# Kernel optimization log

Hardware: AMD Instinct MI355X
Metric: run time of the kernel (lower is better)

The kernel has to match this reference:

```python
import jax, jax.numpy as jnp
import numpy as np

B, V, D, E, F, H, HD = 16, 1024, 16, 64, 16, 128, 64
GRAPH_LAYERS, FLOW_ITERS, DUAL_ITERS = 2, 10, 10
STEP, MOM, BIG = 0.01, 0.9, 1e9


def _build_graph():
    # circulant graph: node v's d-th out-neighbor is v + offs[d] (mod V); offsets paired (o, -o)
    offs = np.array([1, -1, 2, -2, 3, -3, 4, -4, 5, -5, 6, -6, 7, -7, 8, -8], dtype=np.int32)
    v = np.arange(V, dtype=np.int32)[:, None]
    d = np.broadcast_to(np.arange(D, dtype=np.int32)[None, :], (V, D))
    adj = ((v + offs[None, :]) % V).astype(np.int32)
    inv_adj = ((v - offs[None, :]) % V).astype(np.int32)
    in_idx = np.stack([inv_adj, d], axis=-1)    # d-th incoming edge of v == out-edge (inv_adj[v,d], slot d)
    rev_idx = np.stack([adj, d], axis=-1)       # out-edge (v,d) is the d-th incoming edge of adj[v,d]
    opp_idx = np.stack([adj, d ^ 1], axis=-1)   # opposite edge (w->v) is slot d^1 at w (paired offsets)
    bt = lambda x: jnp.asarray(np.broadcast_to(x[None], (B,) + x.shape).copy())
    return bt(adj), bt(inv_adj), bt(in_idx), bt(rev_idx), bt(opp_idx)


def setup_inputs() -> dict:
    key = jax.random.key(0)
    ks = jax.random.split(key, 16)
    adj_lst, inv_adj_lst, in_indices, rev_indices, opp_indices = _build_graph()
    rn = lambda k, shape, scale=1.0: jax.random.normal(k, shape, dtype=jnp.float32) * scale
    s = lambda fan: 1.0 / float(np.sqrt(fan))
    return {
        'demands': rn(ks[0], (B, V, 1)),
        'node_features': rn(ks[1], (B, V, F)),
        'edge_lengths': jax.random.uniform(ks[2], (B, V, D), dtype=jnp.float32),
        'norm_edge_lengths': jax.random.uniform(ks[3], (B, V, D), dtype=jnp.float32),
        'node_emb': rn(ks[4], (V, E)),
        'W_enc': rn(ks[5], (E + F, H), s(E + F)), 'b_enc': jnp.zeros((H,), jnp.float32),
        'W_gat': rn(ks[6], (H, H), s(H)), 'b_gat': jnp.zeros((H,), jnp.float32),
        'a_gat': rn(ks[7], (H,), s(H)),
        'W_gru_x': rn(ks[8], (H, 3 * H), s(H)), 'W_gru_h': rn(ks[9], (H, 3 * H), s(H)),
        'b_gru': jnp.zeros((3 * H,), jnp.float32),
        'W_dec1': rn(ks[10], (2 * H, HD), s(2 * H)), 'b_dec1': jnp.zeros((HD,), jnp.float32),
        'W_dec2': rn(ks[11], (HD, 1), s(HD)), 'b_dec2': jnp.zeros((1,), jnp.float32),
        'W_dual1': rn(ks[12], (H, HD), s(H)), 'b_dual1': jnp.zeros((HD,), jnp.float32),
        'W_dual2': rn(ks[13], (HD, 1), s(HD)), 'b_dual2': jnp.zeros((1,), jnp.float32),
        'adj_lst': adj_lst, 'inv_adj_lst': inv_adj_lst,
        'in_indices': in_indices, 'rev_indices': rev_indices, 'opp_indices': opp_indices,
        'num_nodes': jnp.full((B,), V, dtype=jnp.int32),
    }


def _gather_nodes(values, idx, valid):
    # masked_gather with set_zero=True: values (B,V,H), idx (B,V,D) -> (B,V,D,H)
    bb = jnp.arange(values.shape[0])[:, None, None]
    g = values[bb, jnp.clip(idx, 0, values.shape[1] - 1)]
    return g * valid[..., None]


def _gather_edges(x, idx):
    # gather_nd into a (B,V,D,...) tensor; idx (B,V,D,2) = (node, slot), batch implicit
    bb = jnp.arange(x.shape[0])[:, None, None]
    return x[bb, idx[..., 0], idx[..., 1]]


def _sparsemax(z):
    n = z.shape[-1]
    zs = jnp.sort(z, axis=-1)[..., ::-1]
    k = jnp.arange(1, n + 1, dtype=z.dtype)
    zc = jnp.cumsum(zs, axis=-1)
    support = (1.0 + k * zs) > zc
    kz = jnp.sum(support, axis=-1, keepdims=True)
    tau = (jnp.take_along_axis(zc, kz - 1, axis=-1) - 1.0) / kz.astype(z.dtype)
    return jnp.maximum(z - tau, 0.0)


def _forward(demands, node_features, edge_lengths, norm_edge_lengths, node_emb, W_enc, b_enc,
             W_gat, b_gat, a_gat, W_gru_x, W_gru_h, b_gru, W_dec1, b_dec1, W_dec2, b_dec2,
             W_dual1, b_dual1, W_dual2, b_dual2,
             adj_lst, inv_adj_lst, in_indices, rev_indices, opp_indices, num_nodes):
    f32 = jnp.float32
    # embedding lookup with max_norm=1
    nrm = jnp.linalg.norm(node_emb, axis=-1, keepdims=True)
    emb = node_emb / jnp.maximum(nrm, 1.0)
    emb_b = jnp.broadcast_to(emb[None], (demands.shape[0], V, E))
    node_enc = jnp.concatenate([emb_b, node_features], axis=-1) @ W_enc + b_enc   # (B,V,H)
    mask = (adj_lst == num_nodes[:, None, None]).astype(f32)                       # 1 = padded slot
    valid = 1.0 - mask
    initial = _gather_nodes(node_enc, adj_lst, valid)                              # (B,V,D,H)
    h = initial
    for _ in range(GRAPH_LAYERS):
        # DirectionalGAT: per-edge transform, masked attention over slots, directional regather
        t = jnp.tanh(h @ W_gat + b_gat)                                            # (B,V,D,H)
        logits = jnp.einsum('bvdh,h->bvd', t, a_gat) - BIG * mask
        attn = jax.nn.softmax(logits, axis=-1)
        node_msg = jnp.einsum('bvd,bvdh->bvh', attn, t)                            # (B,V,H)
        msg = _gather_nodes(node_msg, adj_lst, valid)
        x = jnp.tanh(msg + initial)
        # GRU cell, shared weights over all edge states
        gx = x @ W_gru_x + b_gru
        gh = h @ W_gru_h
        z = jax.nn.sigmoid(gx[..., :H] + gh[..., :H])
        r = jax.nn.sigmoid(gx[..., H:2 * H] + gh[..., H:2 * H])
        cand = jnp.tanh(gx[..., 2 * H:] + r * gh[..., 2 * H:])
        h = z * h + (1.0 - z) * cand
    # decoder over (encoding, encoding + opposite-edge encoding)
    comb = h + _gather_edges(h, opp_indices)
    dec_in = jnp.concatenate([h, comb], axis=-1)
    nw = (jnp.tanh(dec_in @ W_dec1 + b_dec1) @ W_dec2 + b_dec2)[..., 0]            # (B,V,D)
    # destination attention: normalize over incoming edges, map back to outgoing layout
    inv_mask = (inv_adj_lst == num_nodes[:, None, None]).astype(f32)
    in_w = _gather_edges(nw, in_indices)
    dest_attn = jax.nn.softmax(in_w - BIG * inv_mask, axis=-1)
    nw = _gather_edges(dest_attn, rev_indices)
    pred = nw - BIG * mask
    normalized = _sparsemax(pred) * valid
    # iterative proportional min-cost-flow solver
    def mcf_step(flow, _):
        inflow = jnp.sum(_gather_edges(flow, in_indices), axis=-1, keepdims=True)  # (B,V,1)
        return normalized * jax.nn.relu(inflow - demands), None
    flow, _ = jax.lax.scan(mcf_step, jnp.zeros_like(normalized), None, length=FLOW_ITERS)
    flow_cost = jnp.sum(flow * flow, axis=(1, 2))                                  # square cost fn
    # dual variables + dual flow (projected momentum gradient descent)
    node_states = jnp.sum(h, axis=2)                                               # (B,V,H)
    dual_vars = jax.nn.relu(jnp.tanh(node_states @ W_dual1 + b_dual1) @ W_dual2 + b_dual2)  # (B,V,1)
    dual = mask * dual_vars
    dual_tr = _gather_nodes(dual_vars, adj_lst, valid)[..., 0]
    dual_diff = dual_tr - dual                                                     # (B,V,D)
    def dual_step(carry, _):
        f, vel = carry
        grad = 2.0 * f + dual_diff                                                 # d/df [f^2 + dual_diff*f]
        vel = MOM * vel - STEP * grad
        f = jax.nn.relu(f + vel)
        return (f, vel), None
    (dual_flows, _), _ = jax.lax.scan(dual_step, (jnp.zeros_like(dual_diff), jnp.zeros_like(dual_diff)), None, length=DUAL_ITERS)
    dual_flows = dual_flows * valid
    dual_demand = jnp.sum(dual_vars * demands, axis=(1, 2))
    dual_cost = jnp.sum(dual_flows * dual_flows + dual_diff * dual_flows, axis=(1, 2)) - dual_demand
    return flow_cost - dual_cost                                                   # (B,) primal-dual gap loss


def reference(demands, node_features, edge_lengths, norm_edge_lengths, node_emb, W_enc, b_enc,
              W_gat, b_gat, a_gat, W_gru_x, W_gru_h, b_gru, W_dec1, b_dec1, W_dec2, b_dec2,
              W_dual1, b_dual1, W_dual2, b_dual2,
              adj_lst, inv_adj_lst, in_indices, rev_indices, opp_indices, num_nodes):
    return _forward(demands, node_features, edge_lengths, norm_edge_lengths, node_emb, W_enc, b_enc,
                    W_gat, b_gat, a_gat, W_gru_x, W_gru_h, b_gru, W_dec1, b_dec1, W_dec2, b_dec2,
                    W_dual1, b_dual1, W_dual2, b_dual2,
                    adj_lst, inv_adj_lst, in_indices, rev_indices, opp_indices, num_nodes)
```

## Files before the change

### kernel.cpp

```cpp
#include <hip/hip_runtime.h>
#include <hip/hip_bf16.h>

#define B 16
#define V 1024
#define D 16
#define E 64
#define F 16
#define H 128
#define HD 64
#define BV (B*V)
#define BVD (B*V*D)

#define OFF_HNB      0
#define OFF_NORM     (OFF_HNB + BV*H/2)
#define OFF_DV       (OFF_NORM + BVD)
#define OFF_WT       (OFF_DV + BV)
#define OFF_WTG      (OFF_WT + 65536)
#define OFF_WPQ      (OFF_WTG + 8192)
#define OFF_WU1T     (OFF_WPQ + 8192)
#define OFF_WENCT    (OFF_WU1T + 4096)

typedef __attribute__((ext_vector_type(8))) short bf16x8;
typedef __attribute__((ext_vector_type(4))) float f32x4;

// ... 9 lines not shown
__device__ __forceinline__ float fsig(float x){ return frcp(1.f + __expf(-x)); }
__device__ __forceinline__ float ftanh(float x){
  float e = __expf(-2.f*fabsf(x));
  float r = (1.f - e)*frcp(1.f + e);
  return copysignf(r, x);
}

__global__ __launch_bounds__(256) void k_pre(const float* __restrict__ Wx, const float* __restrict__ Wh,
    const float* __restrict__ Wg, const float* __restrict__ W1, const float* __restrict__ Wu1,
    const float* __restrict__ Wenc,
    short* __restrict__ Wt, short* __restrict__ Wgt, short* __restrict__ Wpq,
    short* __restrict__ Wu1t, short* __restrict__ Wenct, float* __restrict__ outz){
  int bid = blockIdx.x, tid = threadIdx.x;
  if (bid == 0 && tid < 16) outz[tid] = 0.f;
  if (bid < 512){
    int n = bid, k = tid;
    int g = n >> 7, j = n & 127;
    float v;
    if (g == 0)      v = (k < 128) ? Wx[k*384 + j]       : Wh[(k-128)*384 + j];
    else if (g == 1) v = (k < 128) ? Wx[k*384 + 128 + j] : Wh[(k-128)*384 + 128 + j];
    else if (g == 2) v = (k < 128) ? Wx[k*384 + 256 + j] : 0.f;
    else             v = (k < 128) ? 0.f                 : Wh[(k-128)*384 + 256 + j];
    Wt[n*256 + k] = f2bf(v);
    return;
  }
  if (bid < 576){
    int idx = (bid-512)*256 + tid;
    int n = idx >> 7, k = idx & 127;
    Wgt[n*128 + k] = f2bf(Wg[k*128 + n]);
    return;
  }
  if (bid < 608){
    int idx = (bid-576)*256 + tid;
    int n = idx >> 7, k = idx & 127;
    float wb = W1[(k+128)*HD + n];
    float wa = W1[k*HD + n];
    Wpq[n*128 + k]      = f2bf(wa + wb);
    Wpq[(64+n)*128 + k] = f2bf(wb);
    return;
  }
  if (bid < 640){
    int idx = (bid-608)*256 + tid;
    int n = idx >> 7, k = idx & 127;
    Wu1t[n*128 + k] = f2bf(Wu1[k*HD + n]);
    return;
  }
  {
    int nn = (bid-640)*2 + (tid >> 7);
    int kk = tid & 127;
    if (kk < 96) Wenct[nn*96 + kk] = f2bf(kk < 80 ? Wenc[kk*128 + nn] : 0.f);
  }
}

__global__ __launch_bounds__(512,4) void k_mega(const float* __restrict__ emb, const float* __restrict__ nf,
    const short* __restrict__ Wenct, const float* __restrict__ benc, const int* __restrict__ adj,
    const short* __restrict__ Wgt, const float* __restrict__ bg, const float* __restrict__ ag,
    const short* __restrict__ Wt, const float* __restrict__ bgru, short* __restrict__ hout){
  __shared__ short NE[64][136];
  __shared__ short T[64][136];
  __shared__ short H1[48][136];
  __shared__ short X[48][136];
  __shared__ float Lp[8][64];
  __shared__ float Ls[64];
  __shared__ float nrmv[64];
  short (*As)[136] = T;

  int tid = threadIdx.x;
  int blk = blockIdx.x;
  int b = blk >> 5;
  int n0 = (blk & 31) << 5;
  int w = tid >> 6, lane = tid & 63;
  int l15 = lane & 15, quad = lane >> 4;

  if (tid < 64){
    int v = (n0 - 16 + tid) & 1023;
    const float4* e4 = reinterpret_cast<const float4*>(&emb[v*E]);
    float ss = 0.f;
    #pragma unroll
    for (int q=0;q<16;q++){ float4 x = e4[q]; ss += x.x*x.x + x.y*x.y + x.z*x.z + x.w*x.w; }
    nrmv[tid] = frcp(fmaxf(sqrtf(ss), 1.f));
  }
  __syncthreads();
  for (int e=tid; e<64*16; e+=512){
    int r = e >> 4, q = e & 15;
    int v = (n0 - 16 + r) & 1023;
    float4 x = reinterpret_cast<const float4*>(&emb[v*E])[q];
    float iv = nrmv[r];
    short4 s; s.x=f2bf(x.x*iv); s.y=f2bf(x.y*iv); s.z=f2bf(x.z*iv); s.w=f2bf(x.w*iv);
    *reinterpret_cast<short4*>(&As[r][q*4]) = s;
  }
  for (int e=tid; e<64*4; e+=512){
    int r = e >> 2, q = e & 3;
    int m = (b<<10) + ((n0 - 16 + r) & 1023);
    float4 x = reinterpret_cast<const float4*>(&nf[(long)m*F])[q];
    short4 s; s.x=f2bf(x.x); s.y=f2bf(x.y); s.z=f2bf(x.z); s.w=f2bf(x.w);
    *reinterpret_cast<short4*>(&As[r][64 + q*4]) = s;
    short4 z; z.x=0; z.y=0; z.z=0; z.w=0;
    *reinterpret_cast<short4*>(&As[r][80 + q*4]) = z;
  }
  __syncthreads();
  {
    f32x4 acc[4];
    #pragma unroll
    for (int mt=0;mt<4;mt++) acc[mt] = (f32x4){0.f,0.f,0.f,0.f};
    #pragma unroll
    for (int kc=0;kc<3;kc++){
      int k0 = kc*32;
      bf16x8 bfr = *reinterpret_cast<const bf16x8*>(&Wenct[(16*w + l15)*96 + k0 + quad*8]);
      #pragma unroll
      for (int mt=0;mt<4;mt++){
        bf16x8 a = *reinterpret_cast<const bf16x8*>(&As[16*mt + l15][k0 + quad*8]);
        acc[mt] = __builtin_amdgcn_mfma_f32_16x16x32_bf16(a, bfr, acc[mt], 0,0,0);
      }
    }
    int c = 16*w + l15;
    float bb = benc[c];
    #pragma unroll
    for (int mt=0;mt<4;mt++)
      #pragma unroll
      for (int reg=0;reg<4;reg++)
        NE[16*mt + quad*4 + reg][c] = f2bf(acc[mt][reg] + bb);
  }
  __syncthreads();
  {
    f32x4 acc[4];
    #pragma unroll
    for (int mt=0;mt<4;mt++) acc[mt] = (f32x4){0.f,0.f,0.f,0.f};
    #pragma unroll
    for (int kc=0;kc<4;kc++){
      int k0 = kc*32;
      bf16x8 bfr = *reinterpret_cast<const bf16x8*>(&Wgt[(16*w + l15)*128 + k0 + quad*8]);
      #pragma unroll
      for (int mt=0;mt<4;mt++){
        bf16x8 a = *reinterpret_cast<const bf16x8*>(&NE[16*mt + l15][k0 + quad*8]);
        acc[mt] = __builtin_amdgcn_mfma_f32_16x16x32_bf16(a, bfr, acc[mt], 0,0,0);
      }
    }
    int c = 16*w + l15;
    float bgc = bg[c], agc = ag[c];
    float lp[4][4];
    #pragma unroll
    for (int mt=0;mt<4;mt++)
      #pragma unroll
      for (int reg=0;reg<4;reg++){
        float t = ftanh(acc[mt][reg] + bgc);
        T[16*mt + quad*4 + reg][c] = f2bf(t);
        lp[mt][reg] = t * agc;
      }
    #pragma unroll
    for (int mt=0;mt<4;mt++)
      #pragma unroll
      for (int reg=0;reg<4;reg++){
        lp[mt][reg] += __shfl_xor(lp[mt][reg], 1);
        lp[mt][reg] += __shfl_xor(lp[mt][reg], 2);
        lp[mt][reg] += __shfl_xor(lp[mt][reg], 4);
        lp[mt][reg] += __shfl_xor(lp[mt][reg], 8);
      }
    if (l15 == 0){
      #pragma unroll
      for (int mt=0;mt<4;mt++)
        #pragma unroll
        for (int reg=0;reg<4;reg++)
          Lp[w][16*mt + quad*4 + reg] = lp[mt][reg];
    }
  }
  __syncthreads();
  if (tid < 64){
    float s = 0.f;
    #pragma unroll
    for (int i=0;i<8;i++) s += Lp[i][tid];
    Ls[tid] = s;
  }
  __syncthreads();
  if (tid < 192){
    int vl = tid >> 2, seg = tid & 3;
    int wg = (b<<10) + ((n0 - 8 + vl) & 1023);
    int li[16]; float at[16];
    float m = -1e30f;
    #pragma unroll
    for (int d=0; d<16; d++){
      int a = adj[wg*16 + d];
      li[d] = (a - n0 + 16) & 1023;
      m = fmaxf(m, Ls[li[d]]);
    }
    float s = 0.f;
    #pragma unroll
    for (int d=0; d<16; d++){ at[d] = __expf(Ls[li[d]] - m); s += at[d]; }
    float inv = frcp(s);
    #pragma unroll
    for (int d=0; d<16; d++) at[d] *= inv;
    #pragma unroll
    for (int c8=0; c8<4; c8++){
      int c = seg*32 + c8*8;
      float acc8[8] = {0,0,0,0,0,0,0,0};
      #pragma unroll 4
      for (int d=0; d<16; d++){
        bf16x8 tv = *reinterpret_cast<const bf16x8*>(&T[li[d]][c]);
        float a = at[d];
        #pragma unroll
        for (int q=0;q<8;q++) acc8[q] += a * bf2f(tv[q]);
      }
      bf16x8 nv = *reinterpret_cast<const bf16x8*>(&NE[vl + 8][c]);
      bf16x8 xv;
      #pragma unroll
      for (int q=0;q<8;q++) xv[q] = f2bf(ftanh(acc8[q] + bf2f(nv[q])));
      *reinterpret_cast<bf16x8*>(&X[vl][c]) = xv;
    }
  }
  __syncthreads();
  {
    f32x4 acc[3][4];
    #pragma unroll
    for (int mt=0;mt<3;mt++)
      #pragma unroll
      for (int g=0;g<4;g++) acc[mt][g] = (f32x4){0.f,0.f,0.f,0.f};
    for (int k8=0;k8<8;k8++){
      int k0 = k8*32;
      int gg = (k8 < 4) ? 2 : 3;
      int ncol = 16*w + l15;
      int koff = k0 + quad*8;
      bf16x8 bz = *reinterpret_cast<const bf16x8*>(&Wt[(ncol      )*256 + koff]);
      bf16x8 br = *reinterpret_cast<const bf16x8*>(&Wt[(ncol + 128)*256 + koff]);
      bf16x8 bc = *reinterpret_cast<const bf16x8*>(&Wt[(ncol + gg*128)*256 + koff]);
      #pragma unroll
      for (int mt=0;mt<3;mt++){
        bf16x8 a;
        if (k8 < 4) a = *reinterpret_cast<const bf16x8*>(&X[16*mt + l15][k0 + quad*8]);
        else        a = *reinterpret_cast<const bf16x8*>(&NE[16*mt + l15 + 8][k0 - 128 + quad*8]);
        acc[mt][0]  = __builtin_amdgcn_mfma_f32_16x16x32_bf16(a, bz, acc[mt][0], 0,0,0);
        acc[mt][1]  = __builtin_amdgcn_mfma_f32_16x16x32_bf16(a, br, acc[mt][1], 0,0,0);
        acc[mt][gg] = __builtin_amdgcn_mfma_f32_16x16x32_bf16(a, bc, acc[mt][gg], 0,0,0);
      }
    }
    int j = 16*w + l15;
    float bjz = bgru[j], bjr = bgru[128 + j], bjc = bgru[256 + j];
    #pragma unroll
    for (int mt=0;mt<3;mt++){
      #pragma unroll
      for (int reg=0;reg<4;reg++){
        int rl = 16*mt + quad*4 + reg;
        float z = fsig(acc[mt][0][reg] + bjz);
        float r = fsig(acc[mt][1][reg] + bjr);
        float cand = ftanh(acc[mt][2][reg] + bjc + r*acc[mt][3][reg]);
        float ho = bf2f(NE[rl + 8][j]);
        H1[rl][j] = f2bf(z*ho + (1.f - z)*cand);
      }
    }
  }
  __syncthreads();
  {
    f32x4 acc[3];
    #pragma unroll
    for (int mt=0;mt<3;mt++) acc[mt] = (f32x4){0.f,0.f,0.f,0.f};
    #pragma unroll
    for (int kc=0;kc<4;kc++){
      int k0 = kc*32;
      bf16x8 bfr = *reinterpret_cast<const bf16x8*>(&Wgt[(16*w + l15)*128 + k0 + quad*8]);
      #pragma unroll
      for (int mt=0;mt<3;mt++){
        bf16x8 a = *reinterpret_cast<const bf16x8*>(&H1[16*mt + l15][k0 + quad*8]);
        acc[mt] = __builtin_amdgcn_mfma_f32_16x16x32_bf16(a, bfr, acc[mt], 0,0,0);
      }
    }
    int c = 16*w + l15;
    float bgc = bg[c], agc = ag[c];
    float lp[3][4];
    #pragma unroll
    for (int mt=0;mt<3;mt++)
      #pragma unroll
      for (int reg=0;reg<4;reg++){
        float t = ftanh(acc[mt][reg] + bgc);
        T[16*mt + quad*4 + reg][c] = f2bf(t);
        lp[mt][reg] = t * agc;
      }
    #pragma unroll
    for (int mt=0;mt<3;mt++)
      #pragma unroll
      for (int reg=0;reg<4;reg++){
        lp[mt][reg] += __shfl_xor(lp[mt][reg], 1);
        lp[mt][reg] += __shfl_xor(lp[mt][reg], 2);
        lp[mt][reg] += __shfl_xor(lp[mt][reg], 4);
        lp[mt][reg] += __shfl_xor(lp[mt][reg], 8);
      }
    if (l15 == 0){
      #pragma unroll
      for (int mt=0;mt<3;mt++)
        #pragma unroll
        for (int reg=0;reg<4;reg++)
          Lp[w][16*mt + quad*4 + reg] = lp[mt][reg];
    }
  }
  __syncthreads();
  if (tid < 48){
    float s = 0.f;
    #pragma unroll
    for (int i=0;i<8;i++) s += Lp[i][tid];
    Ls[tid] = s;
  }
  __syncthreads();
  if (tid < 128){
    int vl = tid >> 2, seg = tid & 3;
    int vg = (b<<10) + n0 + vl;
    int li[16]; float at[16];
    float m = -1e30f;
    #pragma unroll
    for (int d=0; d<16; d++){
      int a = adj[vg*16 + d];
      li[d] = (a - n0 + 8) & 1023;
      m = fmaxf(m, Ls[li[d]]);
    }
    float s = 0.f;
    #pragma unroll
    for (int d=0; d<16; d++){ at[d] = __expf(Ls[li[d]] - m); s += at[d]; }
    float inv = frcp(s);
    #pragma unroll
    for (int d=0; d<16; d++) at[d] *= inv;
    #pragma unroll
    for (int c8=0; c8<4; c8++){
      int c = seg*32 + c8*8;
      float acc8[8] = {0,0,0,0,0,0,0,0};
      #pragma unroll 4
      for (int d=0; d<16; d++){
        bf16x8 tv = *reinterpret_cast<const bf16x8*>(&T[li[d]][c]);
        float a = at[d];
        #pragma unroll
        for (int q=0;q<8;q++) acc8[q] += a * bf2f(tv[q]);
      }
      bf16x8 nv = *reinterpret_cast<const bf16x8*>(&NE[vl + 16][c]);
      bf16x8 xv;
      #pragma unroll
      for (int q=0;q<8;q++) xv[q] = f2bf(ftanh(acc8[q] + bf2f(nv[q])));
      *reinterpret_cast<bf16x8*>(&X[vl][c]) = xv;
    }
  }
  __syncthreads();
  {
    f32x4 acc[2][4];
    #pragma unroll
    for (int mt=0;mt<2;mt++)
      #pragma unroll
      for (int g=0;g<4;g++) acc[mt][g] = (f32x4){0.f,0.f,0.f,0.f};
    for (int k8=0;k8<8;k8++){
      int k0 = k8*32;
      int gg = (k8 < 4) ? 2 : 3;
      int ncol = 16*w + l15;
      int koff = k0 + quad*8;
      bf16x8 bz = *reinterpret_cast<const bf16x8*>(&Wt[(ncol      )*256 + koff]);
      bf16x8 br = *reinterpret_cast<const bf16x8*>(&Wt[(ncol + 128)*256 + koff]);
      bf16x8 bc = *reinterpret_cast<const bf16x8*>(&Wt[(ncol + gg*128)*256 + koff]);
      #pragma unroll
      for (int mt=0;mt<2;mt++){
        bf16x8 a;
        if (k8 < 4) a = *reinterpret_cast<const bf16x8*>(&X[16*mt + l15][k0 + quad*8]);
        else        a = *reinterpret_cast<const bf16x8*>(&H1[16*mt + l15 + 8][k0 - 128 + quad*8]);
        acc[mt][0]  = __builtin_amdgcn_mfma_f32_16x16x32_bf16(a, bz, acc[mt][0], 0,0,0);
        acc[mt][1]  = __builtin_amdgcn_mfma_f32_16x16x32_bf16(a, br, acc[mt][1], 0,0,0);
        acc[mt][gg] = __builtin_amdgcn_mfma_f32_16x16x32_bf16(a, bc, acc[mt][gg], 0,0,0);
      }
    }
    __syncthreads();
    int j = 16*w + l15;
    float bjz = bgru[j], bjr = bgru[128 + j], bjc = bgru[256 + j];
    #pragma unroll
    for (int mt=0;mt<2;mt++){
      #pragma unroll
      for (int reg=0;reg<4;reg++){
        int rl = 16*mt + quad*4 + reg;
        float z = fsig(acc[mt][0][reg] + bjz);
        float r = fsig(acc[mt][1][reg] + bjr);
        float cand = ftanh(acc[mt][2][reg] + bjc + r*acc[mt][3][reg]);
        float ho = bf2f(H1[rl + 8][j]);
        X[rl][j] = f2bf(z*ho + (1.f - z)*cand);
      }
    }
  }
  __syncthreads();
  for (int idx=tid; idx<32*16; idx+=512){
    int r = idx >> 4, c8 = idx & 15;
    *reinterpret_cast<bf16x8*>(&hout[(long)((b<<10) + n0 + r)*128 + c8*8]) =
        *reinterpret_cast<const bf16x8*>(&X[r][c8*8]);
  }
}

__global__ __launch_bounds__(512,2) void k_decdas(const short* __restrict__ hn, const int* __restrict__ adj,
    const int* __restrict__ invadj, const short* __restrict__ Wpq, const float* __restrict__ b1,
    const float* __restrict__ W2, const float* __restrict__ b2_,
    const short* __restrict__ Wu1t, const float* __restrict__ bu1, const float* __restrict__ Wu2,
    const float* __restrict__ bu2_, float* __restrict__ norm_, float* __restrict__ dv){
  __shared__ short Hs[112][136];
  __shared__ short PQb[112][132];
  __shared__ short NSs[64][136];
  __shared__ int adjL[64][16];
  __shared__ float dvp[64][4];
  __shared__ float b1s[64], w2s[64], bu1s[64], wu2s[64];
  int tid = threadIdx.x;
  int blk = blockIdx.x;
  int b = blk >> 4;
  int n0 = (blk & 15) << 6;
  if (tid < 64){ b1s[tid] = b1[tid]; w2s[tid] = W2[tid]; bu1s[tid] = bu1[tid]; wu2s[tid] = Wu2[tid]; }
  for (int idx=tid; idx<112*16; idx+=512){
    int r = idx >> 4, c8 = idx & 15;
    int g = (b << 10) + ((n0 - 24 + r) & 1023);
    *reinterpret_cast<bf16x8*>(&Hs[r][c8*8]) =
        *reinterpret_cast<const bf16x8*>(&hn[(long)g*128 + c8*8]);
  }
  for (int idx=tid; idx<1024; idx+=512){
    int r = idx >> 4, d = idx & 15;
    int a = adj[((b<<10) + n0 + r)*16 + d];
    adjL[r][d] = (a - n0 + 24) & 1023;
  }
  __syncthreads();
  int w = tid >> 6, lane = tid & 63;
  int l15 = lane & 15, quad = lane >> 4;
  {
    f32x4 acc[7];
    #pragma unroll
    for (int mt=0;mt<7;mt++) acc[mt] = (f32x4){0.f,0.f,0.f,0.f};
    #pragma unroll
    for (int kc=0;kc<4;kc++){
      int k0 = kc*32;
      bf16x8 bfr = *reinterpret_cast<const bf16x8*>(&Wpq[(16*w + l15)*128 + k0 + quad*8]);
      #pragma unroll
      for (int mt=0;mt<7;mt++){
        bf16x8 a = *reinterpret_cast<const bf16x8*>(&Hs[16*mt + l15][k0 + quad*8]);
        acc[mt] = __builtin_amdgcn_mfma_f32_16x16x32_bf16(a, bfr, acc[mt], 0,0,0);
      }
    }
    int c = 16*w + l15;
    #pragma unroll
    for (int mt=0;mt<7;mt++)
      #pragma unroll
      for (int reg=0;reg<4;reg++)
        PQb[16*mt + quad*4 + reg][c] = f2bf(acc[mt][reg]);
  }
  for (int idx=tid; idx<64*16; idx+=512){
    int r = idx >> 4, c8 = idx & 15;
    float acc8[8] = {0,0,0,0,0,0,0,0};
    #pragma unroll 4
    for (int d=0; d<16; d++){
      bf16x8 hv = *reinterpret_cast<const bf16x8*>(&Hs[adjL[r][d]][c8*8]);
      #pragma unroll
      for (int q=0;q<8;q++) acc8[q] += bf2f(hv[q]);
    }
    bf16x8 sv;
    #pragma unroll
    for (int q=0;q<8;q++) sv[q] = f2bf(acc8[q]);
    *reinterpret_cast<bf16x8*>(&NSs[r][c8*8]) = sv;
  }
  __syncthreads();
  if (w < 4){
    f32x4 acc[4];
    #pragma unroll
    for (int mt=0;mt<4;mt++) acc[mt] = (f32x4){0.f,0.f,0.f,0.f};
    #pragma unroll
    for (int kc=0;kc<4;kc++){
      int k0 = kc*32;
      bf16x8 bfr = *reinterpret_cast<const bf16x8*>(&Wu1t[(16*w + l15)*128 + k0 + quad*8]);
      #pragma unroll
      for (int mt=0;mt<4;mt++){
        bf16x8 a = *reinterpret_cast<const bf16x8*>(&NSs[16*mt + l15][k0 + quad*8]);
        acc[mt] = __builtin_amdgcn_mfma_f32_16x16x32_bf16(a, bfr, acc[mt], 0,0,0);
      }
    }
    int n = 16*w + l15;
    float bn = bu1s[n], wn = wu2s[n];
    #pragma unroll
    for (int mt=0;mt<4;mt++){
      #pragma unroll
      for (int reg=0;reg<4;reg++){
        float p = ftanh(acc[mt][reg] + bn) * wn;
        p += __shfl_xor(p, 1);
        p += __shfl_xor(p, 2);
        p += __shfl_xor(p, 4);
        p += __shfl_xor(p, 8);
        if (l15 == 0) dvp[16*mt + quad*4 + reg][w] = p;
      }
    }
  }
  __syncthreads();
  float* nws = reinterpret_cast<float*>(&Hs[0][0]);
  float b2v = b2_[0];
  for (int e = tid; e < 96*16; e += 512){
    int rr = e >> 4, d = e & 15;
    int wnode = (n0 + rr - 16) & 1023;
    int wg = (b<<10) + wnode;
    int a = adj[wg*16 + d];
    int al = (a - n0 + 24) & 1023;
    int wl = rr + 8;
    float p = 0.f;
    #pragma unroll 8
    for (int c=0;c<64;c++)
      p += ftanh(bf2f(PQb[al][c]) + bf2f(PQb[wl][64 + c]) + b1s[c]) * w2s[c];
    nws[rr*17 + d] = p + b2v;
  }
  __syncthreads();
  if (tid < 64){
    float val = dvp[tid][0]+dvp[tid][1]+dvp[tid][2]+dvp[tid][3];
    dv[(b<<10) + n0 + tid] = fmaxf(val + bu2_[0], 0.f);
  }
  float* datt = reinterpret_cast<float*>(&PQb[0][0]);
  if (tid < 80){
    int wnode = (n0 + tid - 8) & 1023;
    int wg = (b<<10) + wnode;
    float vals[16];
    float m = -1e30f;
    #pragma unroll
    for (int d=0; d<16; d++){
      int iv = invadj[wg*16 + d];
      int il = (iv - n0 + 16) & 1023;
      vals[d] = nws[il*17 + d];
      m = fmaxf(m, vals[d]);
    }
    float s = 0.f;
    #pragma unroll
    for (int d=0; d<16; d++){ vals[d] = __expf(vals[d]-m); s += vals[d]; }
    float inv = frcp(s);
    #pragma unroll
    for (int d=0; d<16; d++) datt[tid*17 + d] = vals[d]*inv;
  }
  __syncthreads();
  if (tid < 64){
    int vg = (b<<10) + n0 + tid;
    float z[16], s[16];
    #pragma unroll
    for (int d=0; d<16; d++){
      int al = adjL[tid][d] - 16;
      z[d] = datt[al*17 + d];
      s[d] = z[d];
    }
    #pragma unroll
    for (int k2 = 2; k2 <= 16; k2 <<= 1){
      #pragma unroll
      for (int jj = k2 >> 1; jj > 0; jj >>= 1){
        #pragma unroll
        for (int i = 0; i < 16; i++){
// ... 88 lines not shown
      float g = 2.f*f + dvv;
      vel = 0.9f*vel - 0.01f*g;
      f = fmaxf(f + vel, 0.f);
    }
    partD = f*f + dvv*f;
    partDD = dvv * dm;
  }
  float val = partF - 16.f*partD + partDD;
  #pragma unroll
  for (int off=32; off>0; off>>=1) val += __shfl_down(val, off);
  if ((tid & 63) == 0) red[tid>>6] = val;
  __syncthreads();
  if (tid == 0) atomicAdd(&out[b], red[0]+red[1]+red[2]+red[3]);
}

extern "C" void kernel_launch(void* const* d_in, const int* in_sizes, int n_in,
                              void* d_out, int out_size, void* d_ws, size_t ws_size,
                              hipStream_t stream){
  (void)in_sizes; (void)n_in; (void)out_size; (void)ws_size;
  const float* demands = (const float*)d_in[0];
  const float* nf      = (const float*)d_in[1];
  const float* emb     = (const float*)d_in[4];
  const float* Wenc    = (const float*)d_in[5];
  const float* benc    = (const float*)d_in[6];
  const float* Wgat    = (const float*)d_in[7];
  const float* bgat    = (const float*)d_in[8];
  const float* agat    = (const float*)d_in[9];
  const float* Wgx     = (const float*)d_in[10];
  const float* Wgh     = (const float*)d_in[11];
  const float* bgru    = (const float*)d_in[12];
  const float* Wd1     = (const float*)d_in[13];
  const float* bd1     = (const float*)d_in[14];
  const float* Wd2     = (const float*)d_in[15];
  const float* bd2     = (const float*)d_in[16];
  const float* Wu1     = (const float*)d_in[17];
  const float* bu1     = (const float*)d_in[18];
  const float* Wu2     = (const float*)d_in[19];
  const float* bu2     = (const float*)d_in[20];
  const int* adj       = (const int*)d_in[21];
  const int* invadj    = (const int*)d_in[22];

  float* ws    = (float*)d_ws;
  short* hnB   = (short*)(ws + OFF_HNB);
  float* nrm   = ws + OFF_NORM;
  float* dv    = ws + OFF_DV;
  short* wt    = (short*)(ws + OFF_WT);
  short* wtg   = (short*)(ws + OFF_WTG);
  short* wpq   = (short*)(ws + OFF_WPQ);
  short* wu1t  = (short*)(ws + OFF_WU1T);
  short* wenct = (short*)(ws + OFF_WENCT);

  k_pre<<<704, 256, 0, stream>>>(Wgx, Wgh, Wgat, Wd1, Wu1, Wenc, wt, wtg, wpq, wu1t, wenct,
                                 (float*)d_out);
  k_mega<<<BV/32, 512, 0, stream>>>(emb, nf, wenct, benc, adj, wtg, bgat, agat, wt, bgru, hnB);
  k_decdas<<<BV/64, 512, 0, stream>>>(hnB, adj, invadj, wpq, bd1, Wd2, bd2,
                                      wu1t, bu1, Wu2, bu2, nrm, dv);
  k_flowfin<<<B*16, 256, 0, stream>>>(nrm, demands, invadj, dv, (float*)d_out);
}
```

Before: 194.4 us.

## Widen mega and decoder blocks to 64 nodes with 1024 threads

k_mega now processes 64 output nodes per block instead of 32, with 1024 threads, so the 16-node halo on each side is a smaller share of the recomputed encoder/GAT/GRU work. Warps are split into column and row-tile groups, and some loops now use one element per thread. k_decdas also moves to 1024 threads with the MFMA row tiles spread across the extra warps. The cost is larger LDS use per block, fewer blocks in the grid (256), and launch_bounds(1024,4) may limit registers or occupancy.

```diff
diff --git a/kernel.cpp b/kernel.cpp
--- a/kernel.cpp
+++ b/kernel.cpp
@@ -85,27 +85,28 @@
   }
 }
 
-__global__ __launch_bounds__(512,4) void k_mega(const float* __restrict__ emb, const float* __restrict__ nf,
+__global__ __launch_bounds__(1024,4) void k_mega(const float* __restrict__ emb, const float* __restrict__ nf,
     const short* __restrict__ Wenct, const float* __restrict__ benc, const int* __restrict__ adj,
     const short* __restrict__ Wgt, const float* __restrict__ bg, const float* __restrict__ ag,
     const short* __restrict__ Wt, const float* __restrict__ bgru, short* __restrict__ hout){
-  __shared__ short NE[64][136];
-  __shared__ short T[64][136];
-  __shared__ short H1[48][136];
-  __shared__ short X[48][136];
-  __shared__ float Lp[8][64];
-  __shared__ float Ls[64];
-  __shared__ float nrmv[64];
-  short (*As)[136] = T;
+  __shared__ short NE[96][136];
+  __shared__ short T[96][136];
+  __shared__ short H1[80][136];
+  __shared__ short X[80][136];
+  __shared__ float Lp[8][96];
+  __shared__ float Ls[96];
+  __shared__ float nrmv[96];
+  short (*As)[104] = reinterpret_cast<short(*)[104]>(&H1[0][0]);
 
   int tid = threadIdx.x;
   int blk = blockIdx.x;
-  int b = blk >> 5;
-  int n0 = (blk & 31) << 5;
+  int b = blk >> 4;
+  int n0 = (blk & 15) << 6;
   int w = tid >> 6, lane = tid & 63;
   int l15 = lane & 15, quad = lane >> 4;
-
-  if (tid < 64){
+  int cw = w & 7, hw = w >> 3;
+
+  if (tid < 96){
     int v = (n0 - 16 + tid) & 1023;
     const float4* e4 = reinterpret_cast<const float4*>(&emb[v*E]);
     float ss = 0.f;
@@ -114,7 +115,7 @@
     nrmv[tid] = frcp(fmaxf(sqrtf(ss), 1.f));
   }
   __syncthreads();
-  for (int e=tid; e<64*16; e+=512){
+  for (int e=tid; e<96*16; e+=1024){
     int r = e >> 4, q = e & 15;
     int v = (n0 - 16 + r) & 1023;
     float4 x = reinterpret_cast<const float4*>(&emb[v*E])[q];
@@ -122,7 +123,7 @@
     short4 s; s.x=f2bf(x.x*iv); s.y=f2bf(x.y*iv); s.z=f2bf(x.z*iv); s.w=f2bf(x.w*iv);
     *reinterpret_cast<short4*>(&As[r][q*4]) = s;
   }
-  for (int e=tid; e<64*4; e+=512){
+  for (int e=tid; e<96*4; e+=1024){
     int r = e >> 2, q = e & 3;
     int m = (b<<10) + ((n0 - 16 + r) & 1023);
     float4 x = reinterpret_cast<const float4*>(&nf[(long)m*F])[q];
@@ -133,80 +134,80 @@
   }
   __syncthreads();
   {
-    f32x4 acc[4];
-    #pragma unroll
-    for (int mt=0;mt<4;mt++) acc[mt] = (f32x4){0.f,0.f,0.f,0.f};
+    f32x4 acc[3];
+    #pragma unroll
+    for (int t=0;t<3;t++) acc[t] = (f32x4){0.f,0.f,0.f,0.f};
     #pragma unroll
     for (int kc=0;kc<3;kc++){
       int k0 = kc*32;
-      bf16x8 bfr = *reinterpret_cast<const bf16x8*>(&Wenct[(16*w + l15)*96 + k0 + quad*8]);
-      #pragma unroll
-      for (int mt=0;mt<4;mt++){
-        bf16x8 a = *reinterpret_cast<const bf16x8*>(&As[16*mt + l15][k0 + quad*8]);
-        acc[mt] = __builtin_amdgcn_mfma_f32_16x16x32_bf16(a, bfr, acc[mt], 0,0,0);
-      }
-    }
-    int c = 16*w + l15;
+      bf16x8 bfr = *reinterpret_cast<const bf16x8*>(&Wenct[(16*cw + l15)*96 + k0 + quad*8]);
+      #pragma unroll
+      for (int t=0;t<3;t++){
+        bf16x8 a = *reinterpret_cast<const bf16x8*>(&As[16*(3*hw+t) + l15][k0 + quad*8]);
+        acc[t] = __builtin_amdgcn_mfma_f32_16x16x32_bf16(a, bfr, acc[t], 0,0,0);
+      }
+    }
+    int c = 16*cw + l15;
     float bb = benc[c];
     #pragma unroll
-    for (int mt=0;mt<4;mt++)
+    for (int t=0;t<3;t++)
       #pragma unroll
       for (int reg=0;reg<4;reg++)
-        NE[16*mt + quad*4 + reg][c] = f2bf(acc[mt][reg] + bb);
-  }
-  __syncthreads();
-  {
-    f32x4 acc[4];
-    #pragma unroll
-    for (int mt=0;mt<4;mt++) acc[mt] = (f32x4){0.f,0.f,0.f,0.f};
+        NE[16*(3*hw+t) + quad*4 + reg][c] = f2bf(acc[t][reg] + bb);
+  }
+  __syncthreads();
+  {
+    f32x4 acc[3];
+    #pragma unroll
+    for (int t=0;t<3;t++) acc[t] = (f32x4){0.f,0.f,0.f,0.f};
     #pragma unroll
     for (int kc=0;kc<4;kc++){
       int k0 = kc*32;
-      bf16x8 bfr = *reinterpret_cast<const bf16x8*>(&Wgt[(16*w + l15)*128 + k0 + quad*8]);
-      #pragma unroll
-      for (int mt=0;mt<4;mt++){
-        bf16x8 a = *reinterpret_cast<const bf16x8*>(&NE[16*mt + l15][k0 + quad*8]);
-        acc[mt] = __builtin_amdgcn_mfma_f32_16x16x32_bf16(a, bfr, acc[mt], 0,0,0);
-      }
-    }
-    int c = 16*w + l15;
+      bf16x8 bfr = *reinterpret_cast<const bf16x8*>(&Wgt[(16*cw + l15)*128 + k0 + quad*8]);
+      #pragma unroll
+      for (int t=0;t<3;t++){
+        bf16x8 a = *reinterpret_cast<const bf16x8*>(&NE[16*(3*hw+t) + l15][k0 + quad*8]);
+        acc[t] = __builtin_amdgcn_mfma_f32_16x16x32_bf16(a, bfr, acc[t], 0,0,0);
+      }
+    }
+    int c = 16*cw + l15;
     float bgc = bg[c], agc = ag[c];
-    float lp[4][4];
-    #pragma unroll
-    for (int mt=0;mt<4;mt++)
+    float lp[3][4];
+    #pragma unroll
+    for (int t=0;t<3;t++)
       #pragma unroll
       for (int reg=0;reg<4;reg++){
-        float t = ftanh(acc[mt][reg] + bgc);
-        T[16*mt + quad*4 + reg][c] = f2bf(t);
-        lp[mt][reg] = t * agc;
-      }
-    #pragma unroll
-    for (int mt=0;mt<4;mt++)
+        float tt = ftanh(acc[t][reg] + bgc);
+        T[16*(3*hw+t) + quad*4 + reg][c] = f2bf(tt);
+        lp[t][reg] = tt * agc;
+      }
+    #pragma unroll
+    for (int t=0;t<3;t++)
       #pragma unroll
       for (int reg=0;reg<4;reg++){
-        lp[mt][reg] += __shfl_xor(lp[mt][reg], 1);
-        lp[mt][reg] += __shfl_xor(lp[mt][reg], 2);
-        lp[mt][reg] += __shfl_xor(lp[mt][reg], 4);
-        lp[mt][reg] += __shfl_xor(lp[mt][reg], 8);
+        lp[t][reg] += __shfl_xor(lp[t][reg], 1);
+        lp[t][reg] += __shfl_xor(lp[t][reg], 2);
+        lp[t][reg] += __shfl_xor(lp[t][reg], 4);
+        lp[t][reg] += __shfl_xor(lp[t][reg], 8);
       }
     if (l15 == 0){
       #pragma unroll
-      for (int mt=0;mt<4;mt++)
+      for (int t=0;t<3;t++)
         #pragma unroll
         for (int reg=0;reg<4;reg++)
-          Lp[w][16*mt + quad*4 + reg] = lp[mt][reg];
-    }
-  }
-  __syncthreads();
-  if (tid < 64){
+          Lp[cw][16*(3*hw+t) + quad*4 + reg] = lp[t][reg];
+    }
+  }
+  __syncthreads();
+  if (tid < 96){
     float s = 0.f;
     #pragma unroll
     for (int i=0;i<8;i++) s += Lp[i][tid];
     Ls[tid] = s;
   }
   __syncthreads();
-  if (tid < 192){
-    int vl = tid >> 2, seg = tid & 3;
+  if (tid < 640){
+    int vl = tid >> 3, seg = tid & 7;
     int wg = (b<<10) + ((n0 - 8 + vl) & 1023);
     int li[16]; float at[16];
     float m = -1e30f;
@@ -223,8 +224,8 @@
     #pragma unroll
     for (int d=0; d<16; d++) at[d] *= inv;
     #pragma unroll
-    for (int c8=0; c8<4; c8++){
-      int c = seg*32 + c8*8;
+    for (int c8=0; c8<2; c8++){
+      int c = seg*16 + c8*8;
       float acc8[8] = {0,0,0,0,0,0,0,0};
       #pragma unroll 4
       for (int d=0; d<16; d++){
@@ -244,39 +245,59 @@
   {
     f32x4 acc[3][4];
     #pragma unroll
-    for (int mt=0;mt<3;mt++)
-      #pragma unroll
-      for (int g=0;g<4;g++) acc[mt][g] = (f32x4){0.f,0.f,0.f,0.f};
-    for (int k8=0;k8<8;k8++){
+    for (int t=0;t<3;t++)
+      #pragma unroll
+      for (int g=0;g<4;g++) acc[t][g] = (f32x4){0.f,0.f,0.f,0.f};
+    int ncol = 16*cw + l15;
+    for (int k8=0;k8<4;k8++){
       int k0 = k8*32;
-      int gg = (k8 < 4) ? 2 : 3;
-      int ncol = 16*w + l15;
       int koff = k0 + quad*8;
       bf16x8 bz = *reinterpret_cast<const bf16x8*>(&Wt[(ncol      )*256 + koff]);
       bf16x8 br = *reinterpret_cast<const bf16x8*>(&Wt[(ncol + 128)*256 + koff]);
-      bf16x8 bc = *reinterpret_cast<const bf16x8*>(&Wt[(ncol + gg*128)*256 + koff]);
-      #pragma unroll
-      for (int mt=0;mt<3;mt++){
-        bf16x8 a;
-        if (k8 < 4) a = *reinterpret_cast<const bf16x8*>(&X[16*mt + l15][k0 + quad*8]);
-        else        a = *reinterpret_cast<const bf16x8*>(&NE[16*mt + l15 + 8][k0 - 128 + quad*8]);
-        acc[mt][0]  = __builtin_amdgcn_mfma_f32_16x16x32_bf16(a, bz, acc[mt][0], 0,0,0);
-        acc[mt][1]  = __builtin_amdgcn_mfma_f32_16x16x32_bf16(a, br, acc[mt][1], 0,0,0);
-        acc[mt][gg] = __builtin_amdgcn_mfma_f32_16x16x32_bf16(a, bc, acc[mt][gg], 0,0,0);
-      }
-    }
-    int j = 16*w + l15;
+      bf16x8 bc = *reinterpret_cast<const bf16x8*>(&Wt[(ncol + 256)*256 + koff]);
+      #pragma unroll
+      for (int t=0;t<3;t++){
+        int mt = 3*hw + t;
+        if (mt < 5){
+          bf16x8 a = *reinterpret_cast<const bf16x8*>(&X[16*mt + l15][k0 + quad*8]);
+          acc[t][0] = __builtin_amdgcn_mfma_f32_16x16x32_bf16(a, bz, acc[t][0], 0,0,0);
+          acc[t][1] = __builtin_amdgcn_mfma_f32_16x16x32_bf16(a, br, acc[t][1], 0,0,0);
+          acc[t][2] = __builtin_amdgcn_mfma_f32_16x16x32_bf16(a, bc, acc[t][2], 0,0,0);
+        }
+      }
+    }
+    for (int k8=4;k8<8;k8++){
+      int k0 = k8*32;
+      int koff = k0 + quad*8;
+      bf16x8 bz = *reinterpret_cast<const bf16x8*>(&Wt[(ncol      )*256 + koff]);
+      bf16x8 br = *reinterpret_cast<const bf16x8*>(&Wt[(ncol + 128)*256 + koff]);
+      bf16x8 bc = *reinterpret_cast<const bf16x8*>(&Wt[(ncol + 384)*256 + koff]);
+      #pragma unroll
+      for (int t=0;t<3;t++){
+        int mt = 3*hw + t;
+        if (mt < 5){
+          bf16x8 a = *reinterpret_cast<const bf16x8*>(&NE[16*mt + l15 + 8][k0 - 128 + quad*8]);
+          acc[t][0] = __builtin_amdgcn_mfma_f32_16x16x32_bf16(a, bz, acc[t][0], 0,0,0);
+          acc[t][1] = __builtin_amdgcn_mfma_f32_16x16x32_bf16(a, br, acc[t][1], 0,0,0);
+          acc[t][3] = __builtin_amdgcn_mfma_f32_16x16x32_bf16(a, bc, acc[t][3], 0,0,0);
+        }
+      }
+    }
+    int j = ncol;
     float bjz = bgru[j], bjr = bgru[128 + j], bjc = bgru[256 + j];
     #pragma unroll
-    for (int mt=0;mt<3;mt++){
-      #pragma unroll
-      for (int reg=0;reg<4;reg++){
-        int rl = 16*mt + quad*4 + reg;
-        float z = fsig(acc[mt][0][reg] + bjz);
-        float r = fsig(acc[mt][1][reg] + bjr);
-        float cand = ftanh(acc[mt][2][reg] + bjc + r*acc[mt][3][reg]);
-        float ho = bf2f(NE[rl + 8][j]);
-        H1[rl][j] = f2bf(z*ho + (1.f - z)*cand);
+    for (int t=0;t<3;t++){
+      int mt = 3*hw + t;
+      if (mt < 5){
+        #pragma unroll
+        for (int reg=0;reg<4;reg++){
+          int rl = 16*mt + quad*4 + reg;
+          float z = fsig(acc[t][0][reg] + bjz);
+          float r = fsig(acc[t][1][reg] + bjr);
+          float cand = ftanh(acc[t][2][reg] + bjc + r*acc[t][3][reg]);
+          float ho = bf2f(NE[rl + 8][j]);
+          H1[rl][j] = f2bf(z*ho + (1.f - z)*cand);
+        }
       }
     }
   }
@@ -284,55 +305,69 @@
   {
     f32x4 acc[3];
     #pragma unroll
-    for (int mt=0;mt<3;mt++) acc[mt] = (f32x4){0.f,0.f,0.f,0.f};
+    for (int t=0;t<3;t++) acc[t] = (f32x4){0.f,0.f,0.f,0.f};
     #pragma unroll
     for (int kc=0;kc<4;kc++){
       int k0 = kc*32;
-      bf16x8 bfr = *reinterpret_cast<const bf16x8*>(&Wgt[(16*w + l15)*128 + k0 + quad*8]);
-      #pragma unroll
-      for (int mt=0;mt<3;mt++){
-        bf16x8 a = *reinterpret_cast<const bf16x8*>(&H1[16*mt + l15][k0 + quad*8]);
-        acc[mt] = __builtin_amdgcn_mfma_f32_16x16x32_bf16(a, bfr, acc[mt], 0,0,0);
-      }
-    }
-    int c = 16*w + l15;
+      bf16x8 bfr = *reinterpret_cast<const bf16x8*>(&Wgt[(16*cw + l15)*128 + k0 + quad*8]);
+      #pragma unroll
+      for (int t=0;t<3;t++){
+        int mt = 3*hw + t;
+        if (mt < 5){
+          bf16x8 a = *reinterpret_cast<const bf16x8*>(&H1[16*mt + l15][k0 + quad*8]);
+          acc[t] = __builtin_amdgcn_mfma_f32_16x16x32_bf16(a, bfr, acc[t], 0,0,0);
+        }
+      }
+    }
+    int c = 16*cw + l15;
     float bgc = bg[c], agc = ag[c];
     float lp[3][4];
     #pragma unroll
-    for (int mt=0;mt<3;mt++)
+    for (int t=0;t<3;t++){
+      int mt = 3*hw + t;
+      if (mt < 5){
+        #pragma unroll
+        for (int reg=0;reg<4;reg++){
+          float tt = ftanh(acc[t][reg] + bgc);
+          T[16*mt + quad*4 + reg][c] = f2bf(tt);
+          lp[t][reg] = tt * agc;
+        }
+      } else {
+        #pragma unroll
+        for (int reg=0;reg<4;reg++) lp[t][reg] = 0.f;
+      }
+    }
+    #pragma unroll
+    for (int t=0;t<3;t++)
       #pragma unroll
       for (int reg=0;reg<4;reg++){
-        float t = ftanh(acc[mt][reg] + bgc);
-        T[16*mt + quad*4 + reg][c] = f2bf(t);
-        lp[mt][reg] = t * agc;
-      }
-    #pragma unroll
-    for (int mt=0;mt<3;mt++)
-      #pragma unroll
-      for (int reg=0;reg<4;reg++){
-        lp[mt][reg] += __shfl_xor(lp[mt][reg], 1);
-        lp[mt][reg] += __shfl_xor(lp[mt][reg], 2);
-        lp[mt][reg] += __shfl_xor(lp[mt][reg], 4);
-        lp[mt][reg] += __shfl_xor(lp[mt][reg], 8);
+        lp[t][reg] += __shfl_xor(lp[t][reg], 1);
+        lp[t][reg] += __shfl_xor(lp[t][reg], 2);
+        lp[t][reg] += __shfl_xor(lp[t][reg], 4);
+        lp[t][reg] += __shfl_xor(lp[t][reg], 8);
       }
     if (l15 == 0){
       #pragma unroll
-      for (int mt=0;mt<3;mt++)
-        #pragma unroll
-        for (int reg=0;reg<4;reg++)
-          Lp[w][16*mt + quad*4 + reg] = lp[mt][reg];
-    }
-  }
-  __syncthreads();
-  if (tid < 48){
+      for (int t=0;t<3;t++){
+        int mt = 3*hw + t;
+        if (mt < 5){
+          #pragma unroll
+          for (int reg=0;reg<4;reg++)
+            Lp[cw][16*mt + quad*4 + reg] = lp[t][reg];
+        }
+      }
+    }
+  }
+  __syncthreads();
+  if (tid < 80){
     float s = 0.f;
     #pragma unroll
     for (int i=0;i<8;i++) s += Lp[i][tid];
     Ls[tid] = s;
   }
   __syncthreads();
-  if (tid < 128){
-    int vl = tid >> 2, seg = tid & 3;
+  {
+    int vl = tid >> 4, seg = tid & 15;
     int vg = (b<<10) + n0 + vl;
     int li[16]; float at[16];
     float m = -1e30f;
@@ -348,74 +383,85 @@
     float inv = frcp(s);
     #pragma unroll
     for (int d=0; d<16; d++) at[d] *= inv;
-    #pragma unroll
-    for (int c8=0; c8<4; c8++){
-      int c = seg*32 + c8*8;
-      float acc8[8] = {0,0,0,0,0,0,0,0};
-      #pragma unroll 4
-      for (int d=0; d<16; d++){
-        bf16x8 tv = *reinterpret_cast<const bf16x8*>(&T[li[d]][c]);
-        float a = at[d];
-        #pragma unroll
-        for (int q=0;q<8;q++) acc8[q] += a * bf2f(tv[q]);
-      }
-      bf16x8 nv = *reinterpret_cast<const bf16x8*>(&NE[vl + 16][c]);
-      bf16x8 xv;
-      #pragma unroll
-      for (int q=0;q<8;q++) xv[q] = f2bf(ftanh(acc8[q] + bf2f(nv[q])));
-      *reinterpret_cast<bf16x8*>(&X[vl][c]) = xv;
-    }
+    int c = seg*8;
+    float acc8[8] = {0,0,0,0,0,0,0,0};
+    #pragma unroll 4
+    for (int d=0; d<16; d++){
+      bf16x8 tv = *reinterpret_cast<const bf16x8*>(&T[li[d]][c]);
+      float a = at[d];
+      #pragma unroll
+      for (int q=0;q<8;q++) acc8[q] += a * bf2f(tv[q]);
+    }
+    bf16x8 nv = *reinterpret_cast<const bf16x8*>(&NE[vl + 16][c]);
+    bf16x8 xv;
+    #pragma unroll
+    for (int q=0;q<8;q++) xv[q] = f2bf(ftanh(acc8[q] + bf2f(nv[q])));
+    *reinterpret_cast<bf16x8*>(&X[vl][c]) = xv;
   }
   __syncthreads();
   {
     f32x4 acc[2][4];
     #pragma unroll
-    for (int mt=0;mt<2;mt++)
-      #pragma unroll
-      for (int g=0;g<4;g++) acc[mt][g] = (f32x4){0.f,0.f,0.f,0.f};
-    for (int k8=0;k8<8;k8++){
+    for (int t=0;t<2;t++)
+      #pragma unroll
+      for (int g=0;g<4;g++) acc[t][g] = (f32x4){0.f,0.f,0.f,0.f};
+    int ncol = 16*cw + l15;
+    for (int k8=0;k8<4;k8++){
       int k0 = k8*32;
-      int gg = (k8 < 4) ? 2 : 3;
-      int ncol = 16*w + l15;
       int koff = k0 + quad*8;
       bf16x8 bz = *reinterpret_cast<const bf16x8*>(&Wt[(ncol      )*256 + koff]);
       bf16x8 br = *reinterpret_cast<const bf16x8*>(&Wt[(ncol + 128)*256 + koff]);
-      bf16x8 bc = *reinterpret_cast<const bf16x8*>(&Wt[(ncol + gg*128)*256 + koff]);
-      #pragma unroll
-      for (int mt=0;mt<2;mt++){
-        bf16x8 a;
-        if (k8 < 4) a = *reinterpret_cast<const bf16x8*>(&X[16*mt + l15][k0 + quad*8]);
-        else        a = *reinterpret_cast<const bf16x8*>(&H1[16*mt + l15 + 8][k0 - 128 + quad*8]);
-        acc[mt][0]  = __builtin_amdgcn_mfma_f32_16x16x32_bf16(a, bz, acc[mt][0], 0,0,0);
-        acc[mt][1]  = __builtin_amdgcn_mfma_f32_16x16x32_bf16(a, br, acc[mt][1], 0,0,0);
-        acc[mt][gg] = __builtin_amdgcn_mfma_f32_16x16x32_bf16(a, bc, acc[mt][gg], 0,0,0);
+      bf16x8 bc = *reinterpret_cast<const bf16x8*>(&Wt[(ncol + 256)*256 + koff]);
+      #pragma unroll
+      for (int t=0;t<2;t++){
+        int mt = 2*hw + t;
+        bf16x8 a = *reinterpret_cast<const bf16x8*>(&X[16*mt + l15][k0 + quad*8]);
+        acc[t][0] = __builtin_amdgcn_mfma_f32_16x16x32_bf16(a, bz, acc[t][0], 0,0,0);
+        acc[t][1] = __builtin_amdgcn_mfma_f32_16x16x32_bf16(a, br, acc[t][1], 0,0,0);
+        acc[t][2] = __builtin_amdgcn_mfma_f32_16x16x32_bf16(a, bc, acc[t][2], 0,0,0);
+      }
+    }
+    for (int k8=4;k8<8;k8++){
+      int k0 = k8*32;
+      int koff = k0 + quad*8;
+      bf16x8 bz = *reinterpret_cast<const bf16x8*>(&Wt[(ncol      )*256 + koff]);
+      bf16x8 br = *reinterpret_cast<const bf16x8*>(&Wt[(ncol + 128)*256 + koff]);
+      bf16x8 bc = *reinterpret_cast<const bf16x8*>(&Wt[(ncol + 384)*256 + koff]);
+      #pragma unroll
+      for (int t=0;t<2;t++){
+        int mt = 2*hw + t;
+        bf16x8 a = *reinterpret_cast<const bf16x8*>(&H1[16*mt + l15 + 8][k0 - 128 + quad*8]);
+        acc[t][0] = __builtin_amdgcn_mfma_f32_16x16x32_bf16(a, bz, acc[t][0], 0,0,0);
+        acc[t][1] = __builtin_amdgcn_mfma_f32_16x16x32_bf16(a, br, acc[t][1], 0,0,0);
+        acc[t][3] = __builtin_amdgcn_mfma_f32_16x16x32_bf16(a, bc, acc[t][3], 0,0,0);
       }
     }
     __syncthreads();
-    int j = 16*w + l15;
+    int j = ncol;
     float bjz = bgru[j], bjr = bgru[128 + j], bjc = bgru[256 + j];
     #pragma unroll
-    for (int mt=0;mt<2;mt++){
+    for (int t=0;t<2;t++){
+      int mt = 2*hw + t;
       #pragma unroll
       for (int reg=0;reg<4;reg++){
         int rl = 16*mt + quad*4 + reg;
-        float z = fsig(acc[mt][0][reg] + bjz);
-        float r = fsig(acc[mt][1][reg] + bjr);
-        float cand = ftanh(acc[mt][2][reg] + bjc + r*acc[mt][3][reg]);
+        float z = fsig(acc[t][0][reg] + bjz);
+        float r = fsig(acc[t][1][reg] + bjr);
+        float cand = ftanh(acc[t][2][reg] + bjc + r*acc[t][3][reg]);
         float ho = bf2f(H1[rl + 8][j]);
         X[rl][j] = f2bf(z*ho + (1.f - z)*cand);
       }
     }
   }
   __syncthreads();
-  for (int idx=tid; idx<32*16; idx+=512){
+  for (int idx=tid; idx<64*16; idx+=1024){
     int r = idx >> 4, c8 = idx & 15;
     *reinterpret_cast<bf16x8*>(&hout[(long)((b<<10) + n0 + r)*128 + c8*8]) =
         *reinterpret_cast<const bf16x8*>(&X[r][c8*8]);
   }
 }
 
-__global__ __launch_bounds__(512,2) void k_decdas(const short* __restrict__ hn, const int* __restrict__ adj,
+__global__ __launch_bounds__(1024,4) void k_decdas(const short* __restrict__ hn, const int* __restrict__ adj,
     const int* __restrict__ invadj, const short* __restrict__ Wpq, const float* __restrict__ b1,
     const float* __restrict__ W2, const float* __restrict__ b2_,
     const short* __restrict__ Wu1t, const float* __restrict__ bu1, const float* __restrict__ Wu2,
@@ -431,43 +477,51 @@
   int b = blk >> 4;
   int n0 = (blk & 15) << 6;
   if (tid < 64){ b1s[tid] = b1[tid]; w2s[tid] = W2[tid]; bu1s[tid] = bu1[tid]; wu2s[tid] = Wu2[tid]; }
-  for (int idx=tid; idx<112*16; idx+=512){
+  for (int idx=tid; idx<112*16; idx+=1024){
     int r = idx >> 4, c8 = idx & 15;
     int g = (b << 10) + ((n0 - 24 + r) & 1023);
     *reinterpret_cast<bf16x8*>(&Hs[r][c8*8]) =
         *reinterpret_cast<const bf16x8*>(&hn[(long)g*128 + c8*8]);
   }
-  for (int idx=tid; idx<1024; idx+=512){
-    int r = idx >> 4, d = idx & 15;
+  {
+    int r = tid >> 4, d = tid & 15;
     int a = adj[((b<<10) + n0 + r)*16 + d];
     adjL[r][d] = (a - n0 + 24) & 1023;
   }
   __syncthreads();
   int w = tid >> 6, lane = tid & 63;
   int l15 = lane & 15, quad = lane >> 4;
-  {
-    f32x4 acc[7];
-    #pragma unroll
-    for (int mt=0;mt<7;mt++) acc[mt] = (f32x4){0.f,0.f,0.f,0.f};
+  int cw = w & 7, hw = w >> 3;
+  {
+    f32x4 acc[4];
+    #pragma unroll
+    for (int t=0;t<4;t++) acc[t] = (f32x4){0.f,0.f,0.f,0.f};
     #pragma unroll
     for (int kc=0;kc<4;kc++){
       int k0 = kc*32;
-      bf16x8 bfr = *reinterpret_cast<const bf16x8*>(&Wpq[(16*w + l15)*128 + k0 + quad*8]);
-      #pragma unroll
-      for (int mt=0;mt<7;mt++){
-        bf16x8 a = *reinterpret_cast<const bf16x8*>(&Hs[16*mt + l15][k0 + quad*8]);
-        acc[mt] = __builtin_amdgcn_mfma_f32_16x16x32_bf16(a, bfr, acc[mt], 0,0,0);
-      }
-    }
-    int c = 16*w + l15;
-    #pragma unroll
-    for (int mt=0;mt<7;mt++)
-      #pragma unroll
-      for (int reg=0;reg<4;reg++)
-        PQb[16*mt + quad*4 + reg][c] = f2bf(acc[mt][reg]);
-  }
-  for (int idx=tid; idx<64*16; idx+=512){
-    int r = idx >> 4, c8 = idx & 15;
+      bf16x8 bfr = *reinterpret_cast<const bf16x8*>(&Wpq[(16*cw + l15)*128 + k0 + quad*8]);
+      #pragma unroll
+      for (int t=0;t<4;t++){
+        int mt = 4*hw + t;
+        if (mt < 7){
+          bf16x8 a = *reinterpret_cast<const bf16x8*>(&Hs[16*mt + l15][k0 + quad*8]);
+          acc[t] = __builtin_amdgcn_mfma_f32_16x16x32_bf16(a, bfr, acc[t], 0,0,0);
+        }
+      }
+    }
+    int c = 16*cw + l15;
+    #pragma unroll
+    for (int t=0;t<4;t++){
+      int mt = 4*hw + t;
+      if (mt < 7){
+        #pragma unroll
+        for (int reg=0;reg<4;reg++)
+          PQb[16*mt + quad*4 + reg][c] = f2bf(acc[t][reg]);
+      }
+    }
+  }
+  {
+    int r = tid >> 4, c8 = tid & 15;
     float acc8[8] = {0,0,0,0,0,0,0,0};
     #pragma unroll 4
     for (int d=0; d<16; d++){
@@ -481,39 +535,40 @@
     *reinterpret_cast<bf16x8*>(&NSs[r][c8*8]) = sv;
   }
   __syncthreads();
-  if (w < 4){
-    f32x4 acc[4];
-    #pragma unroll
-    for (int mt=0;mt<4;mt++) acc[mt] = (f32x4){0.f,0.f,0.f,0.f};
+  if (w < 8){
+    int c4 = w & 3, h2 = w >> 2;
+    f32x4 acc[2];
+    #pragma unroll
+    for (int t=0;t<2;t++) acc[t] = (f32x4){0.f,0.f,0.f,0.f};
     #pragma unroll
     for (int kc=0;kc<4;kc++){
       int k0 = kc*32;
-      bf16x8 bfr = *reinterpret_cast<const bf16x8*>(&Wu1t[(16*w + l15)*128 + k0 + quad*8]);
-      #pragma unroll
-      for (int mt=0;mt<4;mt++){
-        bf16x8 a = *reinterpret_cast<const bf16x8*>(&NSs[16*mt + l15][k0 + quad*8]);
-        acc[mt] = __builtin_amdgcn_mfma_f32_16x16x32_bf16(a, bfr, acc[mt], 0,0,0);
-      }
-    }
-    int n = 16*w + l15;
+      bf16x8 bfr = *reinterpret_cast<const bf16x8*>(&Wu1t[(16*c4 + l15)*128 + k0 + quad*8]);
+      #pragma unroll
+      for (int t=0;t<2;t++){
+        bf16x8 a = *reinterpret_cast<const bf16x8*>(&NSs[16*(2*h2+t) + l15][k0 + quad*8]);
+        acc[t] = __builtin_amdgcn_mfma_f32_16x16x32_bf16(a, bfr, acc[t], 0,0,0);
+      }
+    }
+    int n = 16*c4 + l15;
     float bn = bu1s[n], wn = wu2s[n];
     #pragma unroll
-    for (int mt=0;mt<4;mt++){
+    for (int t=0;t<2;t++){
       #pragma unroll
       for (int reg=0;reg<4;reg++){
-        float p = ftanh(acc[mt][reg] + bn) * wn;
+        float p = ftanh(acc[t][reg] + bn) * wn;
         p += __shfl_xor(p, 1);
         p += __shfl_xor(p, 2);
         p += __shfl_xor(p, 4);
         p += __shfl_xor(p, 8);
-        if (l15 == 0) dvp[16*mt + quad*4 + reg][w] = p;
+        if (l15 == 0) dvp[16*(2*h2+t) + quad*4 + reg][c4] = p;
       }
     }
   }
   __syncthreads();
   float* nws = reinterpret_cast<float*>(&Hs[0][0]);
   float b2v = b2_[0];
-  for (int e = tid; e < 96*16; e += 512){
+  for (int e = tid; e < 96*16; e += 1024){
     int rr = e >> 4, d = e & 15;
     int wnode = (n0 + rr - 16) & 1023;
     int wg = (b<<10) + wnode;
@@ -708,8 +763,8 @@
 
   k_pre<<<704, 256, 0, stream>>>(Wgx, Wgh, Wgat, Wd1, Wu1, Wenc, wt, wtg, wpq, wu1t, wenct,
                                  (float*)d_out);
-  k_mega<<<BV/32, 512, 0, stream>>>(emb, nf, wenct, benc, adj, wtg, bgat, agat, wt, bgru, hnB);
-  k_decdas<<<BV/64, 512, 0, stream>>>(hnB, adj, invadj, wpq, bd1, Wd2, bd2,
-                                      wu1t, bu1, Wu2, bu2, nrm, dv);
+  k_mega<<<BV/64, 1024, 0, stream>>>(emb, nf, wenct, benc, adj, wtg, bgat, agat, wt, bgru, hnB);
+  k_decdas<<<BV/64, 1024, 0, stream>>>(hnB, adj, invadj, wpq, bd1, Wd2, bd2,
+                                       wu1t, bu1, Wu2, bu2, nrm, dv);
   k_flowfin<<<B*16, 256, 0, stream>>>(nrm, demands, invadj, dv, (float*)d_out);
 }
```

After: 203.3 us. 4.5% more time.
